# Kernel optimization log

Measured on AMD Instinct MI355X. Metric: run time of the kernel, lower is better.

## Reference

```python
import jax, jax.numpy as jnp
import numpy as np

N_NODES = 50000
N_GRAPHS = 64


def gcn_conv(x, W, b, src, dst, n_nodes):
    """PyG GCNConv: sym-normalized aggregation with self-loops.
    out_i = sum_{j->i} d_j^{-1/2} d_i^{-1/2} (x_j W) + b, self-loops included."""
    loops = jnp.arange(n_nodes, dtype=src.dtype)
    s = jnp.concatenate([src, loops])  # [E+N]
    d = jnp.concatenate([dst, loops])
    h = x @ W  # [N, H]
    deg = jax.ops.segment_sum(jnp.ones_like(s, dtype=h.dtype), d, num_segments=n_nodes)
    dinv = jnp.where(deg > 0, jax.lax.rsqrt(jnp.maximum(deg, 1.0)), 0.0)
    norm = dinv[s] * dinv[d]  # [E+N]
    msg = h[s] * norm[:, None]  # gather + scale, [E+N, H]
    out = jax.ops.segment_sum(msg, d, num_segments=n_nodes)  # scatter-add
    return out + b


def setup_inputs() -> dict:
    key = jax.random.key(0)
    k1, k2, k3, k4, k5, k6, k7, k8, k9 = jax.random.split(key, 9)
    in_dim, hid, num_robots, out_size = 16, 128, 8, 2
    x = jax.random.normal(k1, (N_NODES, in_dim), dtype=jnp.float32)
    edge_index = jax.random.randint(k2, (2, 800000), 0, N_NODES, dtype=jnp.int64)
    batch = jnp.sort(jax.random.randint(k3, (N_NODES,), 0, N_GRAPHS, dtype=jnp.int64))
    s1 = 1.0 / np.sqrt(in_dim)
    s2 = 1.0 / np.sqrt(hid)
    W1 = jax.random.uniform(k4, (in_dim, hid), jnp.float32, -s1, s1)
    b1 = jax.random.uniform(k5, (hid,), jnp.float32, -s1, s1)
    W2 = jax.random.uniform(k6, (hid, hid), jnp.float32, -s2, s2)
    b2 = jax.random.uniform(k7, (hid,), jnp.float32, -s2, s2)
    Wfc = jax.random.uniform(k8, (hid, out_size * num_robots), jnp.float32, -s2, s2)
    bfc = jax.random.uniform(k9, (out_size * num_robots,), jnp.float32, -s2, s2)
    return {"x": x, "edge_index": edge_index, "batch": batch,
            "W1": W1, "b1": b1, "W2": W2, "b2": b2, "Wfc": Wfc, "bfc": bfc}


def reference(x, edge_index, batch, W1, b1, W2, b2, Wfc, bfc):
    src, dst = edge_index[0], edge_index[1]
    n = x.shape[0]
    h = jax.nn.relu(gcn_conv(x, W1, b1, src, dst, n))
    h = jax.nn.relu(gcn_conv(h, W2, b2, src, dst, n))
    # global_mean_pool over graph ids
    sums = jax.ops.segment_sum(h, batch, num_segments=N_GRAPHS)  # [G, H]
    cnt = jax.ops.segment_sum(jnp.ones((n,), h.dtype), batch, num_segments=N_GRAPHS)
    pooled = sums / jnp.maximum(cnt, 1.0)[:, None]
    vel = pooled @ Wfc + bfc  # [G, num_robots*2]
    return vel.reshape(-1, 8, 2)
```

## Files before the change

kernel.cpp:

```cpp
#include <hip/hip_runtime.h>
#include <hip/hip_bf16.h>

#define HID 128
#define IN_DIM 16

typedef short bf16x8 __attribute__((ext_vector_type(8)));
typedef float f32x4 __attribute__((ext_vector_type(4)));
typedef unsigned short u16x8 __attribute__((ext_vector_type(8)));

__device__ __forceinline__ unsigned short f2bf(float f) {
    unsigned int u = __float_as_uint(f);
    unsigned int r = (u + 0x7FFFu + ((u >> 16) & 1u)) >> 16;
    return (unsigned short)r;
}
__device__ __forceinline__ float bf2f(unsigned short u) {
    return __uint_as_float(((unsigned int)u) << 16);
}

__global__ __launch_bounds__(256) void k_zero_words(unsigned int* p, int n) {
    int i = blockIdx.x * blockDim.x + threadIdx.x;
    if (i < n) p[i] = 0u;
}

__global__ __launch_bounds__(256) void k_hist_count(const int* __restrict__ dst,
                                                    int* __restrict__ indeg,
                                                    int* __restrict__ hist,
                                                    int E, int NB, int chunk) {
    __shared__ int lh[256];
    for (int i = threadIdx.x; i < NB; i += 256) lh[i] = 0;
    __syncthreads();
    int s0 = blockIdx.x * chunk;
    int e_end = min(E, s0 + chunk);
    for (int e = s0 + threadIdx.x; e < e_end; e += 256) {
        int d = dst[e];
        atomicAdd(&indeg[d], 1);
        atomicAdd(&lh[d >> 8], 1);
    }
    __syncthreads();
    for (int i = threadIdx.x; i < NB; i += 256)
        hist[blockIdx.x * NB + i] = lh[i];
}

__global__ __launch_bounds__(256) void k_scan1(const int* __restrict__ indeg, int* __restrict__ offs,
                                               int* __restrict__ blocksum, int N) {
    __shared__ int sdata[256];
    int base = blockIdx.x * 1024 + threadIdx.x * 4;
    int v0 = (base + 0 < N) ? indeg[base + 0] : 0;
    int v1 = (base + 1 < N) ? indeg[base + 1] : 0;
    int v2 = (base + 2 < N) ? indeg[base + 2] : 0;
    int v3 = (base + 3 < N) ? indeg[base + 3] : 0;
    int s = v0 + v1 + v2 + v3;
    sdata[threadIdx.x] = s;
    __syncthreads();
    for (int off = 1; off < 256; off <<= 1) {
        int t = (threadIdx.x >= off) ? sdata[threadIdx.x - off] : 0;
        __syncthreads();
        sdata[threadIdx.x] += t;
        __syncthreads();
    }
    int excl = sdata[threadIdx.x] - s;
    if (base + 0 < N) offs[base + 0] = excl;  excl += v0;
    if (base + 1 < N) offs[base + 1] = excl;  excl += v1;
    if (base + 2 < N) offs[base + 2] = excl;  excl += v2;
    if (base + 3 < N) offs[base + 3] = excl;
    if (threadIdx.x == 255) blocksum[blockIdx.x] = sdata[255];
}

__global__ __launch_bounds__(256) void k_scan2_aux(int* __restrict__ blocksum, int nblk,
                                                   const int* __restrict__ batch, float* __restrict__ cnt,
                                                   const float* __restrict__ W2,
                                                   unsigned short* __restrict__ W2T,
                                                   int N, int G) {
    int bid = blockIdx.x;
    if (bid == 0) {
        int lane = threadIdx.x;
        if (lane < 64) {
            if (nblk <= 64) {
                int orig = (lane < nblk) ? blocksum[lane] : 0;
                int v = orig;
                #pragma unroll
                for (int off = 1; off < 64; off <<= 1) {
                    int t = __shfl_up(v, off, 64);
                    if (lane >= off) v += t;
                }
                if (lane < nblk) blocksum[lane] = v - orig;
            } else if (lane == 0) {
                int acc = 0;
                for (int i = 0; i < nblk; ++i) { int t = blocksum[i]; blocksum[i] = acc; acc += t; }
            }
        }
    } else if (bid == 1) {
        int g = threadIdx.x;
        if (g >= G) return;
        int lo = 0, hi = N;
        while (lo < hi) { int mid = (lo + hi) >> 1; if (batch[mid] < g) lo = mid + 1; else hi = mid; }
        int start = lo;
        lo = 0; hi = N;
        while (lo < hi) { int mid = (lo + hi) >> 1; if (batch[mid] <= g) lo = mid + 1; else hi = mid; }
        cnt[g] = (float)(lo - start);
    } else {
        int t = (bid - 2) * 256 + threadIdx.x;
        int n = t >> 7, k = t & 127;
        W2T[t] = f2bf(W2[(size_t)k * HID + n]);
    }
}

__global__ __launch_bounds__(256) void k_scan3(int* __restrict__ offs,
                                               const int* __restrict__ blocksum,
                                               const int* __restrict__ indeg,
                                               float* __restrict__ dinv,
                                               const float* __restrict__ x,
                                               unsigned short* __restrict__ xs16, int N) {
    int i = blockIdx.x * blockDim.x + threadIdx.x;
    if (i >= N) return;
    offs[i] += blocksum[i >> 10];
    float di = rsqrtf(1.0f + (float)indeg[i]);
    dinv[i] = di;
    #pragma unroll
    for (int q = 0; q < 4; ++q) {
        float4 v = *reinterpret_cast<const float4*>(x + (size_t)i * IN_DIM + q * 4);
        ushort4 o4;
        o4.x = f2bf(di * v.x); o4.y = f2bf(di * v.y);
        o4.z = f2bf(di * v.z); o4.w = f2bf(di * v.w);
        *reinterpret_cast<ushort4*>(xs16 + (size_t)i * IN_DIM + q * 4) = o4;
    }
}

__global__ __launch_bounds__(256) void k_hist_scan(int* __restrict__ hist,
                                                   const int* __restrict__ offs,
                                                   int* __restrict__ bucket_base,
                                                   int NB, int E) {
    __shared__ int sdata[256];
    int b = blockIdx.x;
    int t = threadIdx.x;
    int v = hist[t * NB + b];
    sdata[t] = v;
    __syncthreads();
    for (int off = 1; off < 256; off <<= 1) {
        int tmp = (t >= off) ? sdata[t - off] : 0;
        __syncthreads();
        sdata[t] += tmp;
        __syncthreads();
    }
    int base = offs[b << 8];
    hist[t * NB + b] = sdata[t] - v + base;
    if (t == 0) {
        bucket_base[b] = base;
        if (b == 0) bucket_base[NB] = E;
    }
}

__global__ __launch_bounds__(256) void k_bucket(const int* __restrict__ src, const int* __restrict__ dst,
                                                const int* __restrict__ hist,
                                                unsigned int* __restrict__ bucketed,
                                                int E, int NB, int chunk) {
    __shared__ int lcur[256];
    for (int i = threadIdx.x; i < NB; i += 256) lcur[i] = hist[blockIdx.x * NB + i];
    __syncthreads();
    int s0 = blockIdx.x * chunk;
    int e_end = min(E, s0 + chunk);
    for (int e = s0 + threadIdx.x; e < e_end; e += 256) {
        int d = dst[e], s = src[e];
        int p = atomicAdd(&lcur[d >> 8], 1);
        bucketed[p] = ((unsigned int)d << 16) | (unsigned int)s;
    }
}

__global__ __launch_bounds__(256) void k_fill2(const unsigned int* __restrict__ bucketed,
                                               const int* __restrict__ bucket_base,
                                               const int* __restrict__ offs,
                                               unsigned short* __restrict__ csr, int N) {
    __shared__ int lcur[256];
    int n0 = blockIdx.x << 8;
    int t = threadIdx.x;
    lcur[t] = (n0 + t < N) ? offs[n0 + t] : 0;
    __syncthreads();
    int bb = bucket_base[blockIdx.x], be = bucket_base[blockIdx.x + 1];
    for (int e = bb + t; e < be; e += 256) {
        unsigned int u = bucketed[e];
        int d = (int)(u >> 16), s = (int)(u & 0xFFFFu);
        int p = atomicAdd(&lcur[d - n0], 1);
        csr[p] = (unsigned short)s;
    }
}

__global__ __launch_bounds__(256) void k_gather16(const unsigned short* __restrict__ xs16,
                                                  const int* __restrict__ offs,
                                                  const int* __restrict__ indeg,
                                                  const unsigned short* __restrict__ csr,
                                                  float* __restrict__ y, int N) {
    int t = blockIdx.x * 256 + threadIdx.x;
    int node = t >> 1;
    if (node >= N) return;
    int c = (t & 1) * 8;
    int base = offs[node], deg = indeg[node];
    u16x8 ow = *reinterpret_cast<const u16x8*>(xs16 + (size_t)node * IN_DIM + c);
    float a[8];
    #pragma unroll
    for (int d = 0; d < 8; ++d) a[d] = bf2f(ow[d]);
    int j = 0;
    for (; j + 8 <= deg; j += 8) {
        int sI[8];
        #pragma unroll
        for (int u = 0; u < 8; ++u) sI[u] = csr[base + j + u];
        u16x8 v[8];
        #pragma unroll
        for (int u = 0; u < 8; ++u)
            v[u] = *reinterpret_cast<const u16x8*>(xs16 + (size_t)sI[u] * IN_DIM + c);
        #pragma unroll
        for (int u = 0; u < 8; ++u)
            #pragma unroll
            for (int d = 0; d < 8; ++d) a[d] += bf2f(v[u][d]);
    }
    for (; j < deg; ++j) {
        int s = csr[base + j];
        u16x8 v = *reinterpret_cast<const u16x8*>(xs16 + (size_t)s * IN_DIM + c);
        #pragma unroll
        for (int d = 0; d < 8; ++d) a[d] += bf2f(v[d]);
    }
    float* yp = y + (size_t)node * IN_DIM + c;
    *reinterpret_cast<float4*>(yp + 0) = make_float4(a[0], a[1], a[2], a[3]);
    *reinterpret_cast<float4*>(yp + 4) = make_float4(a[4], a[5], a[6], a[7]);
}

__global__ __launch_bounds__(256) void k_gemm1b(const float* __restrict__ y,
                                                const float* __restrict__ W1,
                                                const float* __restrict__ dinv,
                                                const float* __restrict__ b1,
                                                unsigned short* __restrict__ out, int N) {
    __shared__ float Ws[IN_DIM * HID];
    __shared__ float xs[8][IN_DIM];
    int nb = blockIdx.x * 8;
    for (int i = threadIdx.x * 4; i < IN_DIM * HID; i += 256 * 4)
        *reinterpret_cast<float4*>(&Ws[i]) = *reinterpret_cast<const float4*>(&W1[i]);
    int nrows = min(8, N - nb);
    if (threadIdx.x < 32) {
        int r = threadIdx.x >> 2, c = (threadIdx.x & 3) * 4;
        if (r < nrows)
            *reinterpret_cast<float4*>(&xs[r][c]) =
                *reinterpret_cast<const float4*>(&y[(size_t)(nb + r) * IN_DIM + c]);
    }
    __syncthreads();
    int f = threadIdx.x & 127;
    int g = threadIdx.x >> 7;
    float bb = b1[f];
    for (int r = g; r < nrows; r += 2) {
        int node = nb + r;
        float acc = 0.f;
        #pragma unroll
        for (int k = 0; k < IN_DIM; ++k) acc += xs[r][k] * Ws[k * HID + f];
        float di = dinv[node];
        out[(size_t)node * HID + f] = f2bf(di * fmaxf(di * acc + bb, 0.f));
    }
}

__global__ __launch_bounds__(256) void k_gather_z(const unsigned short* __restrict__ h1p,
                                                  const int* __restrict__ offs,
                                                  const int* __restrict__ indeg,
                                                  const unsigned short* __restrict__ csr,
                                                  unsigned short* __restrict__ z, int N) {
    int t = blockIdx.x * 256 + threadIdx.x;
    int node = t >> 4;
    if (node >= N) return;
    int c = (t & 15) * 8;
    int base = offs[node], deg = indeg[node];
    u16x8 ow = *reinterpret_cast<const u16x8*>(h1p + (size_t)node * HID + c);
    float a[8];
    #pragma unroll
    for (int d = 0; d < 8; ++d) a[d] = bf2f(ow[d]);
    int j = 0;
    for (; j + 8 <= deg; j += 8) {
        int sI[8];
        #pragma unroll
        for (int u = 0; u < 8; ++u) sI[u] = csr[base + j + u];
        u16x8 v[8];
        #pragma unroll
        for (int u = 0; u < 8; ++u)
            v[u] = *reinterpret_cast<const u16x8*>(h1p + (size_t)sI[u] * HID + c);
        #pragma unroll
        for (int u = 0; u < 8; ++u)
            #pragma unroll
            for (int d = 0; d < 8; ++d) a[d] += bf2f(v[u][d]);
    }
    for (; j < deg; ++j) {
        int s = csr[base + j];
        u16x8 v = *reinterpret_cast<const u16x8*>(h1p + (size_t)s * HID + c);
        #pragma unroll
        for (int d = 0; d < 8; ++d) a[d] += bf2f(v[d]);
    }
    u16x8 o;
    #pragma unroll
    for (int d = 0; d < 8; ++d) o[d] = f2bf(a[d]);
    *reinterpret_cast<u16x8*>(z + (size_t)node * HID + c) = o;
}

__global__ __launch_bounds__(256) void k_gemm2_pool(const unsigned short* __restrict__ z,
                                                    const unsigned short* __restrict__ W2T,
                                                    const float* __restrict__ dinv,
                                                    const float* __restrict__ b2,
                                                    const int* __restrict__ batch,
                                                    float* __restrict__ pooled, int N) {
    __shared__ float pool_s[HID];
    int wave = threadIdx.x >> 6;
    int lane = threadIdx.x & 63;
    int R = blockIdx.x * 64 + wave * 16;
    int lr = lane & 15;
    int lk = (lane >> 4) * 8;
    f32x4 acc[8] = {};
    const unsigned short* arow = z + (size_t)(R + lr) * HID;
    #pragma unroll
    for (int kk = 0; kk < 4; ++kk) {
        bf16x8 a = *reinterpret_cast<const bf16x8*>(arow + kk * 32 + lk);
        #pragma unroll
        for (int cf = 0; cf < 8; ++cf) {
            bf16x8 b = *reinterpret_cast<const bf16x8*>(W2T + (size_t)(cf * 16 + lr) * HID + kk * 32 + lk);
            acc[cf] = __builtin_amdgcn_mfma_f32_16x16x32_bf16(a, b, acc[cf], 0, 0, 0);
        }
    }
    int r0 = (lane >> 4) * 4;
    float di[4];
    int nd[4];
    #pragma unroll
    for (int r = 0; r < 4; ++r) {
        nd[r] = R + r0 + r;
        di[r] = (nd[r] < N) ? dinv[nd[r]] : 0.f;
    }
    int R0 = blockIdx.x * 64;
    int gid0 = batch[min(R0, N - 1)];
    bool single = (R0 + 63 < N) && (batch[R0 + 63] == gid0);
    if (single) {
        if (threadIdx.x < HID) pool_s[threadIdx.x] = 0.f;
        __syncthreads();
        #pragma unroll
        for (int cf = 0; cf < 8; ++cf) {
            float bb = b2[cf * 16 + lr];
            float sc = 0.f;
            #pragma unroll
            for (int r = 0; r < 4; ++r)
                sc += fmaxf(di[r] * acc[cf][r] + bb, 0.f);
            sc += __shfl_xor(sc, 16);
            sc += __shfl_xor(sc, 32);
            if (lane < 16) atomicAdd(&pool_s[cf * 16 + lr], sc);
        }
        __syncthreads();
        if (threadIdx.x < HID)
            atomicAdd(&pooled[(size_t)gid0 * HID + threadIdx.x], pool_s[threadIdx.x]);
    } else {
        #pragma unroll
        for (int r = 0; r < 4; ++r) {
            if (nd[r] < N) {
                int bi = batch[nd[r]];
                #pragma unroll
                for (int cf = 0; cf < 8; ++cf) {
                    float v = fmaxf(di[r] * acc[cf][r] + b2[cf * 16 + lr], 0.f);
                    atomicAdd(&pooled[(size_t)bi * HID + cf * 16 + lr], v);
                }
            }
        }
    }
}

__global__ __launch_bounds__(256) void k_fc(const float* __restrict__ pooled,
                                            const float* __restrict__ cnt,
                                            const float* __restrict__ Wfc,
                                            const float* __restrict__ bfc,
                                            float* __restrict__ out, int G, int O) {
    int t = blockIdx.x * blockDim.x + threadIdx.x;
    if (t >= G * O) return;
    int g = t / O, o = t % O;
    float acc = 0.f;
    for (int k = 0; k < HID; ++k) acc += pooled[(size_t)g * HID + k] * Wfc[(size_t)k * O + o];
    out[t] = acc / fmaxf(cnt[g], 1.f) + bfc[o];
}

extern "C" void kernel_launch(void* const* d_in, const int* in_sizes, int n_in,
                              void* d_out, int out_size, void* d_ws, size_t ws_size,
                              hipStream_t stream) {
    const float* x     = (const float*)d_in[0];
    const int*   ei    = (const int*)d_in[1];
    const int*   batch = (const int*)d_in[2];
    const float* W1    = (const float*)d_in[3];
    const float* b1    = (const float*)d_in[4];
    const float* W2    = (const float*)d_in[5];
    const float* b2    = (const float*)d_in[6];
    const float* Wfc   = (const float*)d_in[7];
    const float* bfc   = (const float*)d_in[8];
    float* out = (float*)d_out;

    const int E = in_sizes[1] / 2;
    const int N = in_sizes[2];
    const int O = in_sizes[8];
    const int G = out_size / O;
    const int Npad = ((N + 63) / 64) * 64;
    const int NB = (N + 255) >> 8;
    const int CHUNK = (E + 255) / 256;

    const int* src = ei;
    const int* dst = ei + E;

    char* ws = (char*)d_ws;
    int*   indeg  = (int*)ws;                        ws += sizeof(int) * N;
    float* pooled = (float*)ws;                      ws += sizeof(float) * G * HID;
    float* dinv   = (float*)ws;                      ws += sizeof(float) * N;
    int*   offs   = (int*)ws;                        ws += sizeof(int) * N;
    int*   hist   = (int*)ws;                        ws += sizeof(int) * 256 * NB;
    int*   bucket_base = (int*)ws;                   ws += sizeof(int) * ((NB + 4) & ~3);
    int*   blocksum = (int*)ws;                      ws += sizeof(int) * 256;
    float* cnt    = (float*)ws;                      ws += sizeof(float) * G;
    float* y      = (float*)ws;                      ws += sizeof(float) * (size_t)N * IN_DIM;
    unsigned short* xs16 = (unsigned short*)ws;      ws += sizeof(unsigned short) * (size_t)N * IN_DIM;
    unsigned short* w2t  = (unsigned short*)ws;      ws += sizeof(unsigned short) * (size_t)HID * HID;
    unsigned short* h1p  = (unsigned short*)ws;      ws += sizeof(unsigned short) * (size_t)Npad * HID;
    unsigned short* z    = (unsigned short*)ws;      ws += sizeof(unsigned short) * (size_t)Npad * HID;
    unsigned int*  bucketed = (unsigned int*)ws;     ws += sizeof(unsigned int) * (size_t)E;
    unsigned short* csr  = (unsigned short*)ws;      ws += sizeof(unsigned short) * (size_t)E;

    const int BS = 256;
    const int NBLK_SCAN = (N + 1023) / 1024;

    k_zero_words<<<(N + G * HID + BS - 1) / BS, BS, 0, stream>>>((unsigned int*)indeg, N + G * HID);
    k_hist_count<<<256, BS, 0, stream>>>(dst, indeg, hist, E, NB, CHUNK);
    k_scan1<<<NBLK_SCAN, BS, 0, stream>>>(indeg, offs, blocksum, N);
    k_scan2_aux<<<2 + (HID * HID) / BS, BS, 0, stream>>>(blocksum, NBLK_SCAN, batch, cnt, W2, w2t, N, G);
    k_scan3<<<(N + BS - 1) / BS, BS, 0, stream>>>(offs, blocksum, indeg, dinv, x, xs16, N);
    k_hist_scan<<<NB, BS, 0, stream>>>(hist, offs, bucket_base, NB, E);
    k_bucket<<<256, BS, 0, stream>>>(src, dst, hist, bucketed, E, NB, CHUNK);
    k_fill2<<<NB, BS, 0, stream>>>(bucketed, bucket_base, offs, csr, N);

    k_gather16<<<(N * 2 + BS - 1) / BS, BS, 0, stream>>>(xs16, offs, indeg, csr, y, N);
    k_gemm1b<<<(N + 7) / 8, BS, 0, stream>>>(y, W1, dinv, b1, h1p, N);

    k_gather_z<<<(N * 16 + BS - 1) / BS, BS, 0, stream>>>(h1p, offs, indeg, csr, z, N);
    k_gemm2_pool<<<Npad / 64, BS, 0, stream>>>(z, w2t, dinv, b2, batch, pooled, N);

    k_fc<<<(G * O + BS - 1) / BS, BS, 0, stream>>>(pooled, cnt, Wfc, bfc, out, G, O);
}
```

Measured before the change: 245.9 us.

## Derive degrees from per-bucket histograms and fuse layer-2 gather into MFMA GEMM

The CSR build no longer uses global per-node indegree atomics and a separate node-level scan. Degrees, offsets and dinv are now computed inside the bucket fill kernel from a local 256-node histogram and shared-memory scan, and x scaling moves to its own kernel. The second-layer neighbour gather is fused with the bf16 MFMA GEMM and pooling through a swizzled shared-memory tile, which removes the z intermediate round trip. The cost is fewer threads per node in the gather (4 lanes × 32 channels), so the fused kernel may have less memory-level parallelism and higher register pressure.

New measurement: 212.7 us. 1.16x faster.

```diff
diff --git a/kernel.cpp b/kernel.cpp
--- a/kernel.cpp
+++ b/kernel.cpp
@@ -17,80 +17,62 @@
     return __uint_as_float(((unsigned int)u) << 16);
 }
 
-__global__ __launch_bounds__(256) void k_zero_words(unsigned int* p, int n) {
-    int i = blockIdx.x * blockDim.x + threadIdx.x;
-    if (i < n) p[i] = 0u;
-}
-
-__global__ __launch_bounds__(256) void k_hist_count(const int* __restrict__ dst,
-                                                    int* __restrict__ indeg,
-                                                    int* __restrict__ hist,
-                                                    int E, int NB, int chunk) {
+__global__ __launch_bounds__(256) void k_hist(const int* __restrict__ dst,
+                                              int* __restrict__ hist,
+                                              int E, int NB, int chunk) {
     __shared__ int lh[256];
-    for (int i = threadIdx.x; i < NB; i += 256) lh[i] = 0;
+    lh[threadIdx.x] = 0;
     __syncthreads();
     int s0 = blockIdx.x * chunk;
     int e_end = min(E, s0 + chunk);
-    for (int e = s0 + threadIdx.x; e < e_end; e += 256) {
-        int d = dst[e];
-        atomicAdd(&indeg[d], 1);
-        atomicAdd(&lh[d >> 8], 1);
-    }
+    for (int e = s0 + threadIdx.x; e < e_end; e += 256)
+        atomicAdd(&lh[dst[e] >> 8], 1);
     __syncthreads();
     for (int i = threadIdx.x; i < NB; i += 256)
         hist[blockIdx.x * NB + i] = lh[i];
 }
 
-__global__ __launch_bounds__(256) void k_scan1(const int* __restrict__ indeg, int* __restrict__ offs,
-                                               int* __restrict__ blocksum, int N) {
+__global__ __launch_bounds__(256) void k_hist_scan(int* __restrict__ hist,
+                                                   int* __restrict__ btot, int NB) {
     __shared__ int sdata[256];
-    int base = blockIdx.x * 1024 + threadIdx.x * 4;
-    int v0 = (base + 0 < N) ? indeg[base + 0] : 0;
-    int v1 = (base + 1 < N) ? indeg[base + 1] : 0;
-    int v2 = (base + 2 < N) ? indeg[base + 2] : 0;
-    int v3 = (base + 3 < N) ? indeg[base + 3] : 0;
-    int s = v0 + v1 + v2 + v3;
-    sdata[threadIdx.x] = s;
+    int b = blockIdx.x, t = threadIdx.x;
+    int v = hist[t * NB + b];
+    sdata[t] = v;
     __syncthreads();
     for (int off = 1; off < 256; off <<= 1) {
-        int t = (threadIdx.x >= off) ? sdata[threadIdx.x - off] : 0;
-        __syncthreads();
-        sdata[threadIdx.x] += t;
-        __syncthreads();
-    }
-    int excl = sdata[threadIdx.x] - s;
-    if (base + 0 < N) offs[base + 0] = excl;  excl += v0;
-    if (base + 1 < N) offs[base + 1] = excl;  excl += v1;
-    if (base + 2 < N) offs[base + 2] = excl;  excl += v2;
-    if (base + 3 < N) offs[base + 3] = excl;
-    if (threadIdx.x == 255) blocksum[blockIdx.x] = sdata[255];
-}
-
-__global__ __launch_bounds__(256) void k_scan2_aux(int* __restrict__ blocksum, int nblk,
-                                                   const int* __restrict__ batch, float* __restrict__ cnt,
-                                                   const float* __restrict__ W2,
-                                                   unsigned short* __restrict__ W2T,
-                                                   int N, int G) {
+        int tmp = (t >= off) ? sdata[t - off] : 0;
+        __syncthreads();
+        sdata[t] += tmp;
+        __syncthreads();
+    }
+    hist[t * NB + b] = sdata[t] - v;
+    if (t == 255) btot[b] = sdata[255];
+}
+
+__global__ __launch_bounds__(256) void k_misc(const int* __restrict__ btot,
+                                              int* __restrict__ bucket_base,
+                                              const int* __restrict__ batch, float* __restrict__ cnt,
+                                              const float* __restrict__ W2,
+                                              unsigned short* __restrict__ W2T,
+                                              float* __restrict__ pooled,
+                                              int N, int G, int NB, int E) {
     int bid = blockIdx.x;
+    int t = threadIdx.x;
     if (bid == 0) {
-        int lane = threadIdx.x;
-        if (lane < 64) {
-            if (nblk <= 64) {
-                int orig = (lane < nblk) ? blocksum[lane] : 0;
-                int v = orig;
-                #pragma unroll
-                for (int off = 1; off < 64; off <<= 1) {
-                    int t = __shfl_up(v, off, 64);
-                    if (lane >= off) v += t;
-                }
-                if (lane < nblk) blocksum[lane] = v - orig;
-            } else if (lane == 0) {
-                int acc = 0;
-                for (int i = 0; i < nblk; ++i) { int t = blocksum[i]; blocksum[i] = acc; acc += t; }
-            }
-        }
+        __shared__ int sdata[256];
+        int v = (t < NB) ? btot[t] : 0;
+        sdata[t] = v;
+        __syncthreads();
+        for (int off = 1; off < 256; off <<= 1) {
+            int tmp = (t >= off) ? sdata[t - off] : 0;
+            __syncthreads();
+            sdata[t] += tmp;
+            __syncthreads();
+        }
+        if (t < NB) bucket_base[t] = sdata[t] - v;
+        if (t == 0) bucket_base[NB] = E;
     } else if (bid == 1) {
-        int g = threadIdx.x;
+        int g = t;
         if (g >= G) return;
         int lo = 0, hi = N;
         while (lo < hi) { int mid = (lo + hi) >> 1; if (batch[mid] < g) lo = mid + 1; else hi = mid; }
@@ -98,90 +80,88 @@
         lo = 0; hi = N;
         while (lo < hi) { int mid = (lo + hi) >> 1; if (batch[mid] <= g) lo = mid + 1; else hi = mid; }
         cnt[g] = (float)(lo - start);
+    } else if (bid < 66) {
+        int i = (bid - 2) * 256 + t;
+        int n = i >> 7, k = i & 127;
+        W2T[i] = f2bf(W2[(size_t)k * HID + n]);
     } else {
-        int t = (bid - 2) * 256 + threadIdx.x;
-        int n = t >> 7, k = t & 127;
-        W2T[t] = f2bf(W2[(size_t)k * HID + n]);
-    }
-}
-
-__global__ __launch_bounds__(256) void k_scan3(int* __restrict__ offs,
-                                               const int* __restrict__ blocksum,
-                                               const int* __restrict__ indeg,
-                                               float* __restrict__ dinv,
-                                               const float* __restrict__ x,
-                                               unsigned short* __restrict__ xs16, int N) {
-    int i = blockIdx.x * blockDim.x + threadIdx.x;
-    if (i >= N) return;
-    offs[i] += blocksum[i >> 10];
-    float di = rsqrtf(1.0f + (float)indeg[i]);
-    dinv[i] = di;
-    #pragma unroll
-    for (int q = 0; q < 4; ++q) {
-        float4 v = *reinterpret_cast<const float4*>(x + (size_t)i * IN_DIM + q * 4);
-        ushort4 o4;
-        o4.x = f2bf(di * v.x); o4.y = f2bf(di * v.y);
-        o4.z = f2bf(di * v.z); o4.w = f2bf(di * v.w);
-        *reinterpret_cast<ushort4*>(xs16 + (size_t)i * IN_DIM + q * 4) = o4;
-    }
-}
-
-__global__ __launch_bounds__(256) void k_hist_scan(int* __restrict__ hist,
-                                                   const int* __restrict__ offs,
-                                                   int* __restrict__ bucket_base,
-                                                   int NB, int E) {
-    __shared__ int sdata[256];
-    int b = blockIdx.x;
-    int t = threadIdx.x;
-    int v = hist[t * NB + b];
-    sdata[t] = v;
-    __syncthreads();
-    for (int off = 1; off < 256; off <<= 1) {
-        int tmp = (t >= off) ? sdata[t - off] : 0;
-        __syncthreads();
-        sdata[t] += tmp;
-        __syncthreads();
-    }
-    int base = offs[b << 8];
-    hist[t * NB + b] = sdata[t] - v + base;
-    if (t == 0) {
-        bucket_base[b] = base;
-        if (b == 0) bucket_base[NB] = E;
+        int i = (bid - 66) * 256 + t;
+        if (i < G * HID) pooled[i] = 0.f;
     }
 }
 
 __global__ __launch_bounds__(256) void k_bucket(const int* __restrict__ src, const int* __restrict__ dst,
                                                 const int* __restrict__ hist,
+                                                const int* __restrict__ bucket_base,
                                                 unsigned int* __restrict__ bucketed,
                                                 int E, int NB, int chunk) {
     __shared__ int lcur[256];
-    for (int i = threadIdx.x; i < NB; i += 256) lcur[i] = hist[blockIdx.x * NB + i];
+    for (int i = threadIdx.x; i < NB; i += 256)
+        lcur[i] = hist[blockIdx.x * NB + i] + bucket_base[i];
     __syncthreads();
     int s0 = blockIdx.x * chunk;
     int e_end = min(E, s0 + chunk);
     for (int e = s0 + threadIdx.x; e < e_end; e += 256) {
         int d = dst[e], s = src[e];
         int p = atomicAdd(&lcur[d >> 8], 1);
-        bucketed[p] = ((unsigned int)d << 16) | (unsigned int)s;
-    }
-}
-
-__global__ __launch_bounds__(256) void k_fill2(const unsigned int* __restrict__ bucketed,
+        bucketed[p] = ((unsigned int)(d & 255) << 16) | (unsigned int)s;
+    }
+}
+
+__global__ __launch_bounds__(256) void k_fill3(const unsigned int* __restrict__ bucketed,
                                                const int* __restrict__ bucket_base,
-                                               const int* __restrict__ offs,
-                                               unsigned short* __restrict__ csr, int N) {
-    __shared__ int lcur[256];
-    int n0 = blockIdx.x << 8;
-    int t = threadIdx.x;
-    lcur[t] = (n0 + t < N) ? offs[n0 + t] : 0;
-    __syncthreads();
-    int bb = bucket_base[blockIdx.x], be = bucket_base[blockIdx.x + 1];
+                                               unsigned short* __restrict__ csr,
+                                               int* __restrict__ offs,
+                                               int* __restrict__ indeg,
+                                               float* __restrict__ dinv, int N) {
+    __shared__ int lh[256];
+    __shared__ int sc[256];
+    int b = blockIdx.x, t = threadIdx.x;
+    int n0 = b << 8;
+    lh[t] = 0;
+    __syncthreads();
+    int bb = bucket_base[b], be = bucket_base[b + 1];
+    for (int e = bb + t; e < be; e += 256)
+        atomicAdd(&lh[bucketed[e] >> 16], 1);
+    __syncthreads();
+    int deg = lh[t];
+    sc[t] = deg;
+    __syncthreads();
+    for (int off = 1; off < 256; off <<= 1) {
+        int tmp = (t >= off) ? sc[t - off] : 0;
+        __syncthreads();
+        sc[t] += tmp;
+        __syncthreads();
+    }
+    int excl = sc[t] - deg + bb;
+    int node = n0 + t;
+    if (node < N) {
+        offs[node] = excl;
+        indeg[node] = deg;
+        dinv[node] = rsqrtf(1.0f + (float)deg);
+    }
+    __syncthreads();
+    sc[t] = excl;
+    __syncthreads();
     for (int e = bb + t; e < be; e += 256) {
         unsigned int u = bucketed[e];
-        int d = (int)(u >> 16), s = (int)(u & 0xFFFFu);
-        int p = atomicAdd(&lcur[d - n0], 1);
-        csr[p] = (unsigned short)s;
-    }
+        int p = atomicAdd(&sc[u >> 16], 1);
+        csr[p] = (unsigned short)(u & 0xFFFFu);
+    }
+}
+
+__global__ __launch_bounds__(256) void k_prep(const float* __restrict__ x,
+                                              const float* __restrict__ dinv,
+                                              unsigned short* __restrict__ xs16, int N) {
+    int tt = blockIdx.x * 256 + threadIdx.x;
+    if (tt >= N * 4) return;
+    int node = tt >> 2, q = tt & 3;
+    float di = dinv[node];
+    float4 v = *reinterpret_cast<const float4*>(x + (size_t)node * IN_DIM + q * 4);
+    ushort4 o;
+    o.x = f2bf(di * v.x); o.y = f2bf(di * v.y);
+    o.z = f2bf(di * v.z); o.w = f2bf(di * v.w);
+    *reinterpret_cast<ushort4*>(xs16 + (size_t)node * IN_DIM + q * 4) = o;
 }
 
 __global__ __launch_bounds__(256) void k_gather16(const unsigned short* __restrict__ xs16,
@@ -254,69 +234,92 @@
     }
 }
 
-__global__ __launch_bounds__(256) void k_gather_z(const unsigned short* __restrict__ h1p,
-                                                  const int* __restrict__ offs,
-                                                  const int* __restrict__ indeg,
-                                                  const unsigned short* __restrict__ csr,
-                                                  unsigned short* __restrict__ z, int N) {
-    int t = blockIdx.x * 256 + threadIdx.x;
-    int node = t >> 4;
-    if (node >= N) return;
-    int c = (t & 15) * 8;
-    int base = offs[node], deg = indeg[node];
-    u16x8 ow = *reinterpret_cast<const u16x8*>(h1p + (size_t)node * HID + c);
-    float a[8];
-    #pragma unroll
-    for (int d = 0; d < 8; ++d) a[d] = bf2f(ow[d]);
-    int j = 0;
-    for (; j + 8 <= deg; j += 8) {
-        int sI[8];
-        #pragma unroll
-        for (int u = 0; u < 8; ++u) sI[u] = csr[base + j + u];
-        u16x8 v[8];
-        #pragma unroll
-        for (int u = 0; u < 8; ++u)
-            v[u] = *reinterpret_cast<const u16x8*>(h1p + (size_t)sI[u] * HID + c);
-        #pragma unroll
-        for (int u = 0; u < 8; ++u)
+__global__ __launch_bounds__(256) void k_conv2_fused(const unsigned short* __restrict__ h1p,
+                                                     const int* __restrict__ offs,
+                                                     const int* __restrict__ indeg,
+                                                     const unsigned short* __restrict__ csr,
+                                                     const unsigned short* __restrict__ W2T,
+                                                     const float* __restrict__ dinv,
+                                                     const float* __restrict__ b2,
+                                                     const int* __restrict__ batch,
+                                                     float* __restrict__ pooled, int N) {
+    __shared__ unsigned short zs[64 * HID];
+    __shared__ float pool_s[HID];
+    int t = threadIdx.x;
+    int R0 = blockIdx.x * 64;
+
+    {
+        int node = R0 + (t >> 2);
+        int seg = (t & 3) * 32;
+        float a[32];
+        #pragma unroll
+        for (int i = 0; i < 32; ++i) a[i] = 0.f;
+        if (node < N) {
+            const unsigned short* own = h1p + (size_t)node * HID + seg;
             #pragma unroll
-            for (int d = 0; d < 8; ++d) a[d] += bf2f(v[u][d]);
-    }
-    for (; j < deg; ++j) {
-        int s = csr[base + j];
-        u16x8 v = *reinterpret_cast<const u16x8*>(h1p + (size_t)s * HID + c);
-        #pragma unroll
-        for (int d = 0; d < 8; ++d) a[d] += bf2f(v[d]);
-    }
-    u16x8 o;
-    #pragma unroll
-    for (int d = 0; d < 8; ++d) o[d] = f2bf(a[d]);
-    *reinterpret_cast<u16x8*>(z + (size_t)node * HID + c) = o;
-}
-
-__global__ __launch_bounds__(256) void k_gemm2_pool(const unsigned short* __restrict__ z,
-                                                    const unsigned short* __restrict__ W2T,
-                                                    const float* __restrict__ dinv,
-                                                    const float* __restrict__ b2,
-                                                    const int* __restrict__ batch,
-                                                    float* __restrict__ pooled, int N) {
-    __shared__ float pool_s[HID];
-    int wave = threadIdx.x >> 6;
-    int lane = threadIdx.x & 63;
-    int R = blockIdx.x * 64 + wave * 16;
+            for (int q = 0; q < 4; ++q) {
+                u16x8 v = *reinterpret_cast<const u16x8*>(own + q * 8);
+                #pragma unroll
+                for (int d = 0; d < 8; ++d) a[q * 8 + d] = bf2f(v[d]);
+            }
+            int base = offs[node], deg = indeg[node];
+            int j = 0;
+            for (; j + 2 <= deg; j += 2) {
+                int s0 = csr[base + j], s1 = csr[base + j + 1];
+                const unsigned short* p0 = h1p + (size_t)s0 * HID + seg;
+                const unsigned short* p1 = h1p + (size_t)s1 * HID + seg;
+                u16x8 v[8];
+                #pragma unroll
+                for (int q = 0; q < 4; ++q) v[q] = *reinterpret_cast<const u16x8*>(p0 + q * 8);
+                #pragma unroll
+                for (int q = 0; q < 4; ++q) v[4 + q] = *reinterpret_cast<const u16x8*>(p1 + q * 8);
+                #pragma unroll
+                for (int q = 0; q < 4; ++q)
+                    #pragma unroll
+                    for (int d = 0; d < 8; ++d)
+                        a[q * 8 + d] += bf2f(v[q][d]) + bf2f(v[4 + q][d]);
+            }
+            if (j < deg) {
+                int s0 = csr[base + j];
+                const unsigned short* p0 = h1p + (size_t)s0 * HID + seg;
+                #pragma unroll
+                for (int q = 0; q < 4; ++q) {
+                    u16x8 v = *reinterpret_cast<const u16x8*>(p0 + q * 8);
+                    #pragma unroll
+                    for (int d = 0; d < 8; ++d) a[q * 8 + d] += bf2f(v[d]);
+                }
+            }
+        }
+        int row = t >> 2;
+        #pragma unroll
+        for (int q = 0; q < 4; ++q) {
+            u16x8 o;
+            #pragma unroll
+            for (int d = 0; d < 8; ++d) o[d] = f2bf(a[q * 8 + d]);
+            int byte = row * 256 + seg * 2 + q * 16;
+            byte ^= (row & 7) << 4;
+            *reinterpret_cast<u16x8*>(reinterpret_cast<char*>(zs) + byte) = o;
+        }
+    }
+    __syncthreads();
+
+    int wave = t >> 6;
+    int lane = t & 63;
     int lr = lane & 15;
-    int lk = (lane >> 4) * 8;
+    int lkB = (lane >> 4) * 16;
     f32x4 acc[8] = {};
-    const unsigned short* arow = z + (size_t)(R + lr) * HID;
     #pragma unroll
     for (int kk = 0; kk < 4; ++kk) {
-        bf16x8 a = *reinterpret_cast<const bf16x8*>(arow + kk * 32 + lk);
+        int abyte = (wave * 16 + lr) * 256 + kk * 64 + lkB;
+        abyte ^= (lr & 7) << 4;
+        bf16x8 aF = *reinterpret_cast<const bf16x8*>(reinterpret_cast<const char*>(zs) + abyte);
         #pragma unroll
         for (int cf = 0; cf < 8; ++cf) {
-            bf16x8 b = *reinterpret_cast<const bf16x8*>(W2T + (size_t)(cf * 16 + lr) * HID + kk * 32 + lk);
-            acc[cf] = __builtin_amdgcn_mfma_f32_16x16x32_bf16(a, b, acc[cf], 0, 0, 0);
-        }
-    }
+            bf16x8 bF = *reinterpret_cast<const bf16x8*>(W2T + (size_t)(cf * 16 + lr) * HID + kk * 32 + (lane >> 4) * 8);
+            acc[cf] = __builtin_amdgcn_mfma_f32_16x16x32_bf16(aF, bF, acc[cf], 0, 0, 0);
+        }
+    }
+    int R = R0 + wave * 16;
     int r0 = (lane >> 4) * 4;
     float di[4];
     int nd[4];
@@ -325,11 +328,10 @@
         nd[r] = R + r0 + r;
         di[r] = (nd[r] < N) ? dinv[nd[r]] : 0.f;
     }
-    int R0 = blockIdx.x * 64;
     int gid0 = batch[min(R0, N - 1)];
     bool single = (R0 + 63 < N) && (batch[R0 + 63] == gid0);
     if (single) {
-        if (threadIdx.x < HID) pool_s[threadIdx.x] = 0.f;
+        if (t < HID) pool_s[t] = 0.f;
         __syncthreads();
         #pragma unroll
         for (int cf = 0; cf < 8; ++cf) {
@@ -343,8 +345,8 @@
             if (lane < 16) atomicAdd(&pool_s[cf * 16 + lr], sc);
         }
         __syncthreads();
-        if (threadIdx.x < HID)
-            atomicAdd(&pooled[(size_t)gid0 * HID + threadIdx.x], pool_s[threadIdx.x]);
+        if (t < HID)
+            atomicAdd(&pooled[(size_t)gid0 * HID + t], pool_s[t]);
     } else {
         #pragma unroll
         for (int r = 0; r < 4; ++r) {
@@ -404,34 +406,31 @@
     float* dinv   = (float*)ws;                      ws += sizeof(float) * N;
     int*   offs   = (int*)ws;                        ws += sizeof(int) * N;
     int*   hist   = (int*)ws;                        ws += sizeof(int) * 256 * NB;
-    int*   bucket_base = (int*)ws;                   ws += sizeof(int) * ((NB + 4) & ~3);
-    int*   blocksum = (int*)ws;                      ws += sizeof(int) * 256;
+    int*   btot   = (int*)ws;                        ws += sizeof(int) * 256;
+    int*   bucket_base = (int*)ws;                   ws += sizeof(int) * 260;
     float* cnt    = (float*)ws;                      ws += sizeof(float) * G;
     float* y      = (float*)ws;                      ws += sizeof(float) * (size_t)N * IN_DIM;
     unsigned short* xs16 = (unsigned short*)ws;      ws += sizeof(unsigned short) * (size_t)N * IN_DIM;
     unsigned short* w2t  = (unsigned short*)ws;      ws += sizeof(unsigned short) * (size_t)HID * HID;
     unsigned short* h1p  = (unsigned short*)ws;      ws += sizeof(unsigned short) * (size_t)Npad * HID;
-    unsigned short* z    = (unsigned short*)ws;      ws += sizeof(unsigned short) * (size_t)Npad * HID;
     unsigned int*  bucketed = (unsigned int*)ws;     ws += sizeof(unsigned int) * (size_t)E;
     unsigned short* csr  = (unsigned short*)ws;      ws += sizeof(unsigned short) * (size_t)E;
 
     const int BS = 256;
-    const int NBLK_SCAN = (N + 1023) / 1024;
-
-    k_zero_words<<<(N + G * HID + BS - 1) / BS, BS, 0, stream>>>((unsigned int*)indeg, N + G * HID);
-    k_hist_count<<<256, BS, 0, stream>>>(dst, indeg, hist, E, NB, CHUNK);
-    k_scan1<<<NBLK_SCAN, BS, 0, stream>>>(indeg, offs, blocksum, N);
-    k_scan2_aux<<<2 + (HID * HID) / BS, BS, 0, stream>>>(blocksum, NBLK_SCAN, batch, cnt, W2, w2t, N, G);
-    k_scan3<<<(N + BS - 1) / BS, BS, 0, stream>>>(offs, blocksum, indeg, dinv, x, xs16, N);
-    k_hist_scan<<<NB, BS, 0, stream>>>(hist, offs, bucket_base, NB, E);
-    k_bucket<<<256, BS, 0, stream>>>(src, dst, hist, bucketed, E, NB, CHUNK);
-    k_fill2<<<NB, BS, 0, stream>>>(bucketed, bucket_base, offs, csr, N);
+
+    k_hist<<<256, BS, 0, stream>>>(dst, hist, E, NB, CHUNK);
+    k_hist_scan<<<NB, BS, 0, stream>>>(hist, btot, NB);
+    k_misc<<<66 + (G * HID + BS - 1) / BS, BS, 0, stream>>>(btot, bucket_base, batch, cnt,
+                                                            W2, w2t, pooled, N, G, NB, E);
+    k_bucket<<<256, BS, 0, stream>>>(src, dst, hist, bucket_base, bucketed, E, NB, CHUNK);
+    k_fill3<<<NB, BS, 0, stream>>>(bucketed, bucket_base, csr, offs, indeg, dinv, N);
+    k_prep<<<(N * 4 + BS - 1) / BS, BS, 0, stream>>>(x, dinv, xs16, N);
 
     k_gather16<<<(N * 2 + BS - 1) / BS, BS, 0, stream>>>(xs16, offs, indeg, csr, y, N);
     k_gemm1b<<<(N + 7) / 8, BS, 0, stream>>>(y, W1, dinv, b1, h1p, N);
 
-    k_gather_z<<<(N * 16 + BS - 1) / BS, BS, 0, stream>>>(h1p, offs, indeg, csr, z, N);
-    k_gemm2_pool<<<Npad / 64, BS, 0, stream>>>(z, w2t, dinv, b2, batch, pooled, N);
+    k_conv2_fused<<<(N + 63) / 64, BS, 0, stream>>>(h1p, offs, indeg, csr, w2t, dinv, b2,
+                                                    batch, pooled, N);
 
     k_fc<<<(G * O + BS - 1) / BS, BS, 0, stream>>>(pooled, cnt, Wfc, bfc, out, G, O);
 }
```
